# Performance work log

Measured on AMD Instinct MI355X. Metric: run time of the kernel, lower is better.

Reference implementation:

```python
import jax, jax.numpy as jnp
import numpy as np

N_NODES = 50000
N_EDGES = 500000
IN_DIM = 256
HEADS = 4
OUT_C = 64
NEG_SLOPE = 0.2


def setup_inputs() -> dict:
    key = jax.random.key(0)
    ks = jax.random.split(key, 6)
    x = jax.random.normal(ks[0], (N_NODES, IN_DIM), dtype=jnp.float32)
    edge_index = jax.random.randint(ks[1], (2, N_EDGES), 0, N_NODES, dtype=jnp.int64)
    scale = 1.0 / np.sqrt(IN_DIM)
    W_l = jax.random.normal(ks[2], (IN_DIM, HEADS * OUT_C), dtype=jnp.float32) * scale
    W_r = jax.random.normal(ks[3], (IN_DIM, HEADS * OUT_C), dtype=jnp.float32) * scale
    b_l = jnp.zeros((HEADS * OUT_C,), dtype=jnp.float32)
    b_r = jnp.zeros((HEADS * OUT_C,), dtype=jnp.float32)
    att = jax.random.normal(ks[4], (HEADS, OUT_C), dtype=jnp.float32) * (1.0 / np.sqrt(OUT_C))
    bias = jnp.zeros((HEADS * OUT_C,), dtype=jnp.float32)
    return {"x": x, "edge_index": edge_index, "W_l": W_l, "b_l": b_l,
            "W_r": W_r, "b_r": b_r, "att": att, "bias": bias}


def _gatv2(x, edge_index, W_l, b_l, W_r, b_r, att, bias):
    N = x.shape[0]
    H, C = att.shape
    # add self loops (PyG GATv2Conv default add_self_loops=True)
    loop = jnp.arange(N, dtype=edge_index.dtype)
    src = jnp.concatenate([edge_index[0], loop])  # message sources (x_j)
    dst = jnp.concatenate([edge_index[1], loop])  # aggregation targets (x_i)
    x_l = (x @ W_l + b_l).reshape(N, H, C)  # source-side projection
    x_r = (x @ W_r + b_r).reshape(N, H, C)  # target-side projection
    # GATv2 attention logits: a^T LeakyReLU(x_l[src] + x_r[dst])
    e = jax.nn.leaky_relu(x_l[src] + x_r[dst], NEG_SLOPE)  # [E, H, C]
    logits = jnp.einsum('ehc,hc->eh', e, att)              # [E, H]
    # segmented softmax over incoming edges of each dst node
    m = jax.ops.segment_max(logits, dst, num_segments=N)   # [N, H]
    ex = jnp.exp(logits - m[dst])
    denom = jax.ops.segment_sum(ex, dst, num_segments=N)   # [N, H]
    alpha = ex / denom[dst]                                # [E, H]
    # weighted scatter-aggregation of source messages
    out = jax.ops.segment_sum(x_l[src] * alpha[:, :, None], dst, num_segments=N)  # [N, H, C]
    return out.reshape(N, H * C) + bias


def reference(x, edge_index, W_l, b_l, W_r, b_r, att, bias):
    out = _gatv2(x, edge_index, W_l, b_l, W_r, b_r, att, bias)  # [N, H*C]
    # wrapper: single relation -> reshape(-1, 1, output_dim) and cat on dim=1
    return out.reshape(-1, 1, HEADS * OUT_C)
```

## Files before the change

### kernel.cpp

```cpp
#include <hip/hip_runtime.h>
#include <hip/hip_bf16.h>
#include <math.h>

#define N_NODES 50000
#define N_PAD   50048
#define N_EDGES 500000
#define E_TOT   550000
#define HC      256
#define NHC     512
#define HEADS   4
#define NEG     0.2f

typedef __attribute__((ext_vector_type(8))) short short8;
typedef __attribute__((ext_vector_type(4))) float f32x4;
typedef __attribute__((ext_vector_type(2))) float f32x2;

__device__ __forceinline__ ushort f2bf(float f) {
    union { float f; unsigned u; } c; c.f = f;
    unsigned u = c.u;
    unsigned rounded = u + 0x7FFFu + ((u >> 16) & 1u);
    return (ushort)(rounded >> 16);
}

static constexpr size_t OFF_COUNTS = 0;
static constexpr size_t OFF_CUR    = OFF_COUNTS + (size_t)N_NODES * 4;
static constexpr size_t OFF_ROWS   = OFF_CUR + (size_t)N_NODES * 4;
static constexpr size_t OFF_SRCS   = OFF_ROWS + (size_t)(N_NODES + 1) * 4;
static constexpr size_t OFF_BSUM   = OFF_SRCS + (size_t)E_TOT * 4;
static constexpr size_t OFF_MODE   = OFF_BSUM + 64 * 4;
static constexpr size_t OFF_XB     = ((OFF_MODE + 4 + 255) / 256) * 256;
static constexpr size_t OFF_WT     = OFF_XB + (size_t)N_PAD * HC * 2;
static constexpr size_t OFF_XLB    = OFF_WT + (size_t)NHC * HC * 2;
static constexpr size_t OFF_XRB    = OFF_XLB + (size_t)N_NODES * HC * 2;

__device__ __forceinline__ int get_src(const int* __restrict__ ei, int mode, int e) {
    if (e >= N_EDGES) return e - N_EDGES;
    return mode ? ei[2 * e] : ei[e];
}
__device__ __forceinline__ int get_dst(const int* __restrict__ ei, int mode, int e) {
    if (e >= N_EDGES) return e - N_EDGES;
    return mode ? ei[2 * (N_EDGES + e)] : ei[N_EDGES + e];
}

#define XBLK 6256
#define WBLK 512
#define ZBLK 98
__global__ __launch_bounds__(256) void prep_kernel(
        const float* __restrict__ x, const float* __restrict__ Wl,
        const float* __restrict__ Wr, const int* __restrict__ ei,
        ushort* __restrict__ xb, ushort* __restrict__ wt,
        int* __restrict__ cz, int* __restrict__ mode) {
    const int b = blockIdx.x;
    if (b < XBLK) {
        size_t i = ((size_t)b * 256 + threadIdx.x) * 8;
        if (i >= (size_t)N_PAD * HC) return;
        ushort o[8];
        if (i < (size_t)N_NODES * HC) {
            float4 v0 = *(const float4*)(x + i);
            float4 v1 = *(const float4*)(x + i + 4);
            o[0] = f2bf(v0.x); o[1] = f2bf(v0.y); o[2] = f2bf(v0.z); o[3] = f2bf(v0.w);
            o[4] = f2bf(v1.x); o[5] = f2bf(v1.y); o[6] = f2bf(v1.z); o[7] = f2bf(v1.w);
        } else {
#pragma unroll
            for (int j = 0; j < 8; ++j) o[j] = 0;
        }
        *(short8*)(xb + i) = *(short8*)o;
    } else if (b < XBLK + WBLK) {
        int i = (b - XBLK) * 256 + threadIdx.x;
        int n = i >> 8, k = i & 255;
        float v = (n < HC) ? Wl[(size_t)k * HC + n] : Wr[(size_t)k * HC + (n - HC)];
        wt[i] = f2bf(v);
    } else if (b < XBLK + WBLK + ZBLK) {
        int i4 = (b - XBLK - WBLK) * 256 + threadIdx.x;
        if (i4 < 2 * N_NODES / 4) *(int4*)(cz + i4 * 4) = make_int4(0, 0, 0, 0);
    } else {
        __shared__ int any;
        if (threadIdx.x == 0) any = 0;
        __syncthreads();
        if (ei[2 * threadIdx.x + 1] != 0) atomicOr(&any, 1);
        __syncthreads();
        if (threadIdx.x == 0) mode[0] = (any == 0) ? 1 : 0;
    }
}

#define BM 128
#define BK 32
#define GEMM_BLKS 1564
#define CNT_BLKS  2149
__global__ __launch_bounds__(256) void gemm_count_kernel(
        const __hip_bfloat16* __restrict__ xb, const __hip_bfloat16* __restrict__ wt,
        const float* __restrict__ bl, const float* __restrict__ br,
        ushort* __restrict__ xlb, ushort* __restrict__ xrb,
        const int* __restrict__ ei, const int* __restrict__ mode,
        int* __restrict__ counts) {
    __shared__ ushort smem[4 * BM * BK];

    if (blockIdx.x >= GEMM_BLKS) {
        int e = (blockIdx.x - GEMM_BLKS) * 256 + threadIdx.x;
        if (e < E_TOT) atomicAdd(&counts[get_dst(ei, *mode, e)], 1);
        return;
    }

    auto AS = [&](int buf) { return (__hip_bfloat16*)(smem + buf * BM * BK); };
    auto BS = [&](int buf) { return (__hip_bfloat16*)(smem + 2 * BM * BK + buf * BM * BK); };
    const int t    = threadIdx.x;
    const int lane = t & 63;
    const int wid  = t >> 6;
    const int wr   = wid >> 1, wc = wid & 1;

    const int orig = blockIdx.x;
    const int xcd  = orig & 7;
    const int base = (xcd < 4) ? xcd * 196 : 784 + (xcd - 4) * 195;
    const int work = base + (orig >> 3);
    const int bx   = work >> 2, by = work & 3;
    const int brow = bx * BM;
    const int bcol = by * BM;

    auto stage = [&](int buf, int k0) {
#pragma unroll
        for (int r = 0; r < 2; ++r) {
            int c = r * 256 + t;
            const __hip_bfloat16* ga = xb + ((size_t)(brow + (c >> 2)) * HC + k0 + (c & 3) * 8);
            __builtin_amdgcn_global_load_lds(
                (const __attribute__((address_space(1))) void*)ga,
                (__attribute__((address_space(3))) void*)((char*)AS(buf) + c * 16),
                16, 0, 0);
        }
#pragma unroll
        for (int r = 0; r < 2; ++r) {
            int c = r * 256 + t;
            const __hip_bfloat16* gb2 = wt + ((size_t)(bcol + (c >> 2)) * HC + k0 + (c & 3) * 8);
            __builtin_amdgcn_global_load_lds(
                (const __attribute__((address_space(1))) void*)gb2,
                (__attribute__((address_space(3))) void*)((char*)BS(buf) + c * 16),
                16, 0, 0);
        }
    };

    f32x4 acc[4][4];
#pragma unroll
    for (int m = 0; m < 4; ++m)
#pragma unroll
        for (int n = 0; n < 4; ++n) acc[m][n] = (f32x4)0.f;

    stage(0, 0);
    __syncthreads();

    const int rsub = lane & 15;
    const int koff = (lane >> 4) * 16;

    for (int kk = 0; kk < 8; ++kk) {
        const int cur = kk & 1;
        if (kk < 7) stage(cur ^ 1, (kk + 1) * BK);
        short8 a[4], b[4];
#pragma unroll
        for (int m = 0; m < 4; ++m)
            a[m] = *(const short8*)((const char*)AS(cur) +
                    (wr * 64 + m * 16 + rsub) * (BK * 2) + koff);
#pragma unroll
        for (int n = 0; n < 4; ++n)
            b[n] = *(const short8*)((const char*)BS(cur) +
                    (wc * 64 + n * 16 + rsub) * (BK * 2) + koff);
#pragma unroll
        for (int m = 0; m < 4; ++m)
#pragma unroll
            for (int n = 0; n < 4; ++n)
                acc[m][n] = __builtin_amdgcn_mfma_f32_16x16x32_bf16(a[m], b[n], acc[m][n], 0, 0, 0);
        __syncthreads();
    }

    ushort* dst = (bcol < HC) ? xlb : xrb;
    const float* bvec = (bcol < HC) ? bl : br;
    const int cb = bcol & (HC - 1);
#pragma unroll
    for (int m = 0; m < 4; ++m) {
#pragma unroll
        for (int n = 0; n < 4; ++n) {
            int c_loc = wc * 64 + n * 16 + (lane & 15);
            float bv = bvec[cb + c_loc];
#pragma unroll
            for (int j = 0; j < 4; ++j) {
                int r_loc = wr * 64 + m * 16 + (lane >> 4) * 4 + j;
                smem[r_loc * 128 + (((c_loc >> 3) ^ (r_loc & 15)) * 8) + (c_loc & 7)] =
                    f2bf(acc[m][n][j] + bv);
            }
        }
    }
    __syncthreads();
    {
        const int r = t >> 1, hf = t & 1;
        if (brow + r < N_NODES) {
            ushort* gout = dst + (size_t)(brow + r) * HC + cb + hf * 64;
#pragma unroll
            for (int i = 0; i < 8; ++i) {
                int ci = hf * 8 + i;
                uint4 v = *(const uint4*)&smem[r * 128 + ((ci ^ (r & 15)) * 8)];
                *(uint4*)(gout + i * 8) = v;
            }
        }
    }
}

__global__ void scan1_kernel(const int* __restrict__ counts, int* __restrict__ rows,
                             int* __restrict__ bsum) {
    __shared__ int sdata[256];
    const int t = threadIdx.x;
    const int base = blockIdx.x * 1024 + t * 4;
    int v[4]; int s = 0;
#pragma unroll
    for (int j = 0; j < 4; ++j) {
        int idx = base + j;
        v[j] = (idx < N_NODES) ? counts[idx] : 0;
        s += v[j];
    }
    sdata[t] = s;
    __syncthreads();
    for (int off = 1; off < 256; off <<= 1) {
        int xv = (t >= off) ? sdata[t - off] : 0;
        __syncthreads();
        sdata[t] += xv;
        __syncthreads();
    }
    int run = sdata[t] - s;
#pragma unroll
    for (int j = 0; j < 4; ++j) {
        int idx = base + j;
        if (idx < N_NODES) rows[idx] = run;
        run += v[j];
    }
    if (t == 255) bsum[blockIdx.x] = sdata[255];
}

__global__ void scan3_kernel(int* __restrict__ rows, const int* __restrict__ bsum) {
    const int idx = blockIdx.x * 256 + threadIdx.x;
    const int r = blockIdx.x >> 2;
    const int lane = threadIdx.x & 63;
    int v = (lane < r) ? bsum[lane] : 0;
#pragma unroll
    for (int off = 1; off < 64; off <<= 1) v += __shfl_xor(v, off, 64);
    if (idx < N_NODES) rows[idx] += v;
    if (idx == 0) rows[N_NODES] = E_TOT;
}

__global__ void fill_kernel(const int* __restrict__ ei, const int* __restrict__ mode,
                            const int* __restrict__ rows, int* __restrict__ cursor,
                            int* __restrict__ srcs) {
    int e = blockIdx.x * blockDim.x + threadIdx.x;
    if (e < E_TOT) {
        int md = *mode;
        int d = get_dst(ei, md, e);
        int s = get_src(ei, md, e);
        int pos = atomicAdd(&cursor[d], 1);
        srcs[rows[d] + pos] = s;
    }
}

__global__ __launch_bounds__(256) void fused_agg_kernel(
        const ushort* __restrict__ xlb, const ushort* __restrict__ xrb,
        const float* __restrict__ att,
        const int* __restrict__ rows, const int* __restrict__ srcs,
        const float* __restrict__ bias, float* __restrict__ out) {
    const int lane = threadIdx.x & 63;
    const int n = (blockIdx.x * 256 + threadIdx.x) >> 6;
    if (n >= N_NODES) return;
    const int half = lane >> 5;
    const int sl   = lane & 31;
    const int start = rows[n], end = rows[n + 1];

    f32x2 xr2[4], at2[4];
    {
        uint4 c = *(const uint4*)(xrb + (size_t)n * HC + sl * 8);
        unsigned w[4] = {c.x, c.y, c.z, c.w};
#pragma unroll
        for (int j = 0; j < 4; ++j) {
            xr2[j][0] = __uint_as_float(w[j] << 16);
            xr2[j][1] = __uint_as_float(w[j] & 0xffff0000u);
        }
        float4 a0 = *(const float4*)&att[sl * 8];
        float4 a1 = *(const float4*)&att[sl * 8 + 4];
        at2[0][0] = a0.x; at2[0][1] = a0.y; at2[1][0] = a0.z; at2[1][1] = a0.w;
        at2[2][0] = a1.x; at2[2][1] = a1.y; at2[3][0] = a1.z; at2[3][1] = a1.w;
    }

    f32x2 acc2[4];
#pragma unroll
    for (int j = 0; j < 4; ++j) acc2[j] = (f32x2)0.f;
    float sm = 0.f;

    int i = start + half;
    uint4 rA = make_uint4(0, 0, 0, 0);
    int sB = -1;
    if (i < end) rA = *(const uint4*)(xlb + (size_t)srcs[i] * HC + sl * 8);
    if (i + 2 < end) sB = srcs[i + 2];

    for (; i < end; i += 2) {
        uint4 r = rA;
        if (sB >= 0) rA = *(const uint4*)(xlb + (size_t)sB * HC + sl * 8);
        sB = (i + 4 < end) ? srcs[i + 4] : -1;

        unsigned w[4] = {r.x, r.y, r.z, r.w};
        f32x2 xv[4];
#pragma unroll
        for (int j = 0; j < 4; ++j) {
            xv[j][0] = __uint_as_float(w[j] << 16);
            xv[j][1] = __uint_as_float(w[j] & 0xffff0000u);
        }

        f32x2 p2 = (f32x2)0.f;
#pragma unroll
        for (int j = 0; j < 4; ++j) {
            f32x2 v = xv[j] + xr2[j];
            f32x2 lk = __builtin_elementwise_max(v, v * NEG);
            p2 = lk * at2[j] + p2;
        }
        float p = p2[0] + p2[1];
        p += __shfl_xor(p, 1, 64);
        p += __shfl_xor(p, 2, 64);
        p += __shfl_xor(p, 4, 64);

        float wgt = __expf(p);
        sm += wgt;
        f32x2 w2; w2[0] = wgt; w2[1] = wgt;
#pragma unroll
        for (int j = 0; j < 4; ++j) acc2[j] = xv[j] * w2 + acc2[j];
    }

    sm += __shfl_xor(sm, 32, 64);
#pragma unroll
    for (int j = 0; j < 4; ++j) {
        acc2[j][0] += __shfl_xor(acc2[j][0], 32, 64);
        acc2[j][1] += __shfl_xor(acc2[j][1], 32, 64);
    }

    if (half == 0) {
        const float inv = 1.0f / sm;
        float4 b0 = *(const float4*)&bias[sl * 8];
        float4 b1 = *(const float4*)&bias[sl * 8 + 4];
        float4 o0, o1;
        o0.x = fmaf(acc2[0][0], inv, b0.x); o0.y = fmaf(acc2[0][1], inv, b0.y);
        o0.z = fmaf(acc2[1][0], inv, b0.z); o0.w = fmaf(acc2[1][1], inv, b0.w);
        o1.x = fmaf(acc2[2][0], inv, b1.x); o1.y = fmaf(acc2[2][1], inv, b1.y);
        o1.z = fmaf(acc2[3][0], inv, b1.z); o1.w = fmaf(acc2[3][1], inv, b1.w);
        *(float4*)&out[(size_t)n * HC + sl * 8]     = o0;
        *(float4*)&out[(size_t)n * HC + sl * 8 + 4] = o1;
    }
}

extern "C" void kernel_launch(void* const* d_in, const int* in_sizes, int n_in,
                              void* d_out, int out_size, void* d_ws, size_t ws_size,
                              hipStream_t stream) {
    const float* x    = (const float*)d_in[0];
    const int*   ei   = (const int*)d_in[1];
    const float* Wl   = (const float*)d_in[2];
    const float* bl   = (const float*)d_in[3];
    const float* Wr   = (const float*)d_in[4];
    const float* br   = (const float*)d_in[5];
    const float* att  = (const float*)d_in[6];
    const float* bias = (const float*)d_in[7];
    float* out = (float*)d_out;

    char* ws = (char*)d_ws;
    int*   counts = (int*)(ws + OFF_COUNTS);
    int*   cursor = (int*)(ws + OFF_CUR);
    int*   rows   = (int*)(ws + OFF_ROWS);
    int*   srcs   = (int*)(ws + OFF_SRCS);
    int*   bsum   = (int*)(ws + OFF_BSUM);
    int*   mode   = (int*)(ws + OFF_MODE);
    ushort* xb    = (ushort*)(ws + OFF_XB);
    ushort* wt    = (ushort*)(ws + OFF_WT);
    ushort* xlb   = (ushort*)(ws + OFF_XLB);
    ushort* xrb   = (ushort*)(ws + OFF_XRB);

    prep_kernel<<<XBLK + WBLK + ZBLK + 1, 256, 0, stream>>>(
        x, Wl, Wr, ei, xb, wt, counts, mode);

    gemm_count_kernel<<<GEMM_BLKS + CNT_BLKS, 256, 0, stream>>>(
        (const __hip_bfloat16*)xb, (const __hip_bfloat16*)wt, bl, br, xlb, xrb,
        ei, mode, counts);

    scan1_kernel<<<49, 256, 0, stream>>>(counts, rows, bsum);
    scan3_kernel<<<(N_NODES + 255) / 256, 256, 0, stream>>>(rows, bsum);

    fill_kernel<<<(E_TOT + 255) / 256, 256, 0, stream>>>(ei, mode, rows, cursor, srcs);

    fused_agg_kernel<<<(N_NODES + 3) / 4, 256, 0, stream>>>(
        xlb, xrb, att, rows, srcs, bias, out);
}
```

Measured before the change: 149.0 us.

## Fuse fp32-to-bf16 conversion of x into GEMM A-tile staging

Removes the separate pass that converted x to a padded bf16 buffer. The GEMM now loads fp32 x directly into registers, converts to bf16, and writes to LDS after the MFMA step, software-pipelined one k-step ahead. This avoids writing and re-reading an intermediate bf16 copy of x. The cost is more global bytes read by the GEMM and losing the async global_load_lds path for the A tile.

Result: slower. 152.3 us (+2.2%).

```diff
diff --git a/kernel.cpp b/kernel.cpp
--- a/kernel.cpp
+++ b/kernel.cpp
@@ -28,8 +28,7 @@
 static constexpr size_t OFF_SRCS   = OFF_ROWS + (size_t)(N_NODES + 1) * 4;
 static constexpr size_t OFF_BSUM   = OFF_SRCS + (size_t)E_TOT * 4;
 static constexpr size_t OFF_MODE   = OFF_BSUM + 64 * 4;
-static constexpr size_t OFF_XB     = ((OFF_MODE + 4 + 255) / 256) * 256;
-static constexpr size_t OFF_WT     = OFF_XB + (size_t)N_PAD * HC * 2;
+static constexpr size_t OFF_WT     = ((OFF_MODE + 4 + 255) / 256) * 256;
 static constexpr size_t OFF_XLB    = OFF_WT + (size_t)NHC * HC * 2;
 static constexpr size_t OFF_XRB    = OFF_XLB + (size_t)N_NODES * HC * 2;
 
@@ -42,36 +41,20 @@
     return mode ? ei[2 * (N_EDGES + e)] : ei[N_EDGES + e];
 }
 
-#define XBLK 6256
 #define WBLK 512
 #define ZBLK 98
 __global__ __launch_bounds__(256) void prep_kernel(
-        const float* __restrict__ x, const float* __restrict__ Wl,
-        const float* __restrict__ Wr, const int* __restrict__ ei,
-        ushort* __restrict__ xb, ushort* __restrict__ wt,
-        int* __restrict__ cz, int* __restrict__ mode) {
+        const float* __restrict__ Wl, const float* __restrict__ Wr,
+        const int* __restrict__ ei,
+        ushort* __restrict__ wt, int* __restrict__ cz, int* __restrict__ mode) {
     const int b = blockIdx.x;
-    if (b < XBLK) {
-        size_t i = ((size_t)b * 256 + threadIdx.x) * 8;
-        if (i >= (size_t)N_PAD * HC) return;
-        ushort o[8];
-        if (i < (size_t)N_NODES * HC) {
-            float4 v0 = *(const float4*)(x + i);
-            float4 v1 = *(const float4*)(x + i + 4);
-            o[0] = f2bf(v0.x); o[1] = f2bf(v0.y); o[2] = f2bf(v0.z); o[3] = f2bf(v0.w);
-            o[4] = f2bf(v1.x); o[5] = f2bf(v1.y); o[6] = f2bf(v1.z); o[7] = f2bf(v1.w);
-        } else {
-#pragma unroll
-            for (int j = 0; j < 8; ++j) o[j] = 0;
-        }
-        *(short8*)(xb + i) = *(short8*)o;
-    } else if (b < XBLK + WBLK) {
-        int i = (b - XBLK) * 256 + threadIdx.x;
+    if (b < WBLK) {
+        int i = b * 256 + threadIdx.x;
         int n = i >> 8, k = i & 255;
         float v = (n < HC) ? Wl[(size_t)k * HC + n] : Wr[(size_t)k * HC + (n - HC)];
         wt[i] = f2bf(v);
-    } else if (b < XBLK + WBLK + ZBLK) {
-        int i4 = (b - XBLK - WBLK) * 256 + threadIdx.x;
+    } else if (b < WBLK + ZBLK) {
+        int i4 = (b - WBLK) * 256 + threadIdx.x;
         if (i4 < 2 * N_NODES / 4) *(int4*)(cz + i4 * 4) = make_int4(0, 0, 0, 0);
     } else {
         __shared__ int any;
@@ -88,7 +71,7 @@
 #define GEMM_BLKS 1564
 #define CNT_BLKS  2149
 __global__ __launch_bounds__(256) void gemm_count_kernel(
-        const __hip_bfloat16* __restrict__ xb, const __hip_bfloat16* __restrict__ wt,
+        const float* __restrict__ x, const __hip_bfloat16* __restrict__ wt,
         const float* __restrict__ bl, const float* __restrict__ br,
         ushort* __restrict__ xlb, ushort* __restrict__ xrb,
         const int* __restrict__ ei, const int* __restrict__ mode,
@@ -116,16 +99,29 @@
     const int brow = bx * BM;
     const int bcol = by * BM;
 
-    auto stage = [&](int buf, int k0) {
-#pragma unroll
-        for (int r = 0; r < 2; ++r) {
-            int c = r * 256 + t;
-            const __hip_bfloat16* ga = xb + ((size_t)(brow + (c >> 2)) * HC + k0 + (c & 3) * 8);
-            __builtin_amdgcn_global_load_lds(
-                (const __attribute__((address_space(1))) void*)ga,
-                (__attribute__((address_space(3))) void*)((char*)AS(buf) + c * 16),
-                16, 0, 0);
-        }
+    float4 aLo0, aHi0, aLo1, aHi1;
+    auto loadA = [&](int k0) {
+        const int c0 = t, c1 = 256 + t;
+        int row0 = brow + (c0 >> 2), row1 = brow + (c1 >> 2);
+        if (row0 < N_NODES) {
+            const float* p = x + (size_t)row0 * HC + k0 + (c0 & 3) * 8;
+            aLo0 = *(const float4*)p; aHi0 = *(const float4*)(p + 4);
+        } else { aLo0 = make_float4(0,0,0,0); aHi0 = make_float4(0,0,0,0); }
+        if (row1 < N_NODES) {
+            const float* p = x + (size_t)row1 * HC + k0 + (c1 & 3) * 8;
+            aLo1 = *(const float4*)p; aHi1 = *(const float4*)(p + 4);
+        } else { aLo1 = make_float4(0,0,0,0); aHi1 = make_float4(0,0,0,0); }
+    };
+    auto writeA = [&](int buf) {
+        ushort o[8];
+        o[0]=f2bf(aLo0.x); o[1]=f2bf(aLo0.y); o[2]=f2bf(aLo0.z); o[3]=f2bf(aLo0.w);
+        o[4]=f2bf(aHi0.x); o[5]=f2bf(aHi0.y); o[6]=f2bf(aHi0.z); o[7]=f2bf(aHi0.w);
+        *(short8*)((char*)AS(buf) + t * 16) = *(short8*)o;
+        o[0]=f2bf(aLo1.x); o[1]=f2bf(aLo1.y); o[2]=f2bf(aLo1.z); o[3]=f2bf(aLo1.w);
+        o[4]=f2bf(aHi1.x); o[5]=f2bf(aHi1.y); o[6]=f2bf(aHi1.z); o[7]=f2bf(aHi1.w);
+        *(short8*)((char*)AS(buf) + (256 + t) * 16) = *(short8*)o;
+    };
+    auto stageB = [&](int buf, int k0) {
 #pragma unroll
         for (int r = 0; r < 2; ++r) {
             int c = r * 256 + t;
@@ -143,7 +139,9 @@
 #pragma unroll
         for (int n = 0; n < 4; ++n) acc[m][n] = (f32x4)0.f;
 
-    stage(0, 0);
+    loadA(0);
+    writeA(0);
+    stageB(0, 0);
     __syncthreads();
 
     const int rsub = lane & 15;
@@ -151,7 +149,10 @@
 
     for (int kk = 0; kk < 8; ++kk) {
         const int cur = kk & 1;
-        if (kk < 7) stage(cur ^ 1, (kk + 1) * BK);
+        if (kk < 7) {
+            loadA((kk + 1) * BK);
+            stageB(cur ^ 1, (kk + 1) * BK);
+        }
         short8 a[4], b[4];
 #pragma unroll
         for (int m = 0; m < 4; ++m)
@@ -166,6 +167,7 @@
 #pragma unroll
             for (int n = 0; n < 4; ++n)
                 acc[m][n] = __builtin_amdgcn_mfma_f32_16x16x32_bf16(a[m], b[n], acc[m][n], 0, 0, 0);
+        if (kk < 7) writeA(cur ^ 1);
         __syncthreads();
     }
 
@@ -366,17 +368,14 @@
     int*   srcs   = (int*)(ws + OFF_SRCS);
     int*   bsum   = (int*)(ws + OFF_BSUM);
     int*   mode   = (int*)(ws + OFF_MODE);
-    ushort* xb    = (ushort*)(ws + OFF_XB);
     ushort* wt    = (ushort*)(ws + OFF_WT);
     ushort* xlb   = (ushort*)(ws + OFF_XLB);
     ushort* xrb   = (ushort*)(ws + OFF_XRB);
 
-    prep_kernel<<<XBLK + WBLK + ZBLK + 1, 256, 0, stream>>>(
-        x, Wl, Wr, ei, xb, wt, counts, mode);
+    prep_kernel<<<WBLK + ZBLK + 1, 256, 0, stream>>>(Wl, Wr, ei, wt, counts, mode);
 
     gemm_count_kernel<<<GEMM_BLKS + CNT_BLKS, 256, 0, stream>>>(
-        (const __hip_bfloat16*)xb, (const __hip_bfloat16*)wt, bl, br, xlb, xrb,
-        ei, mode, counts);
+        x, (const __hip_bfloat16*)wt, bl, br, xlb, xrb, ei, mode, counts);
 
     scan1_kernel<<<49, 256, 0, stream>>>(counts, rows, bsum);
     scan3_kernel<<<(N_NODES + 255) / 256, 256, 0, stream>>>(rows, bsum);
```
